# Kernel optimization log

Measured on AMD Instinct MI355X. Metric: run time of the kernel, lower is better.

Reference implementation:

```python
import jax, jax.numpy as jnp
import numpy as np

N = 50000       # num nodes
E = 400000      # num edges (before self loops)
IN, HID, H, OUT = 128, 64, 4, 64
SLOPE = 0.2     # PyG GATv2Conv default negative_slope


def setup_inputs() -> dict:
    key = jax.random.key(0)
    ks = jax.random.split(key, 14)
    def lin(k, fan_in, fan_out):
        return jax.random.normal(k, (fan_in, fan_out), jnp.float32) / np.sqrt(fan_in)
    return {
        "x": jax.random.normal(ks[0], (N, IN), jnp.float32),
        "edge_index": jax.random.randint(ks[1], (2, E), 0, N, jnp.int32),
        # layer 1: in=IN -> HID per head, H heads, concat
        "Wl1": lin(ks[2], IN, H * HID), "bl1": jnp.zeros((H * HID,), jnp.float32),
        "Wr1": lin(ks[3], IN, H * HID), "br1": jnp.zeros((H * HID,), jnp.float32),
        "att1": jax.random.normal(ks[4], (H, HID), jnp.float32) / np.sqrt(HID),
        "bias1": jnp.zeros((H * HID,), jnp.float32),
        # layer 2: in=H*HID -> OUT, 1 head, concat=False
        "Wl2": lin(ks[5], H * HID, OUT), "bl2": jnp.zeros((OUT,), jnp.float32),
        "Wr2": lin(ks[6], H * HID, OUT), "br2": jnp.zeros((OUT,), jnp.float32),
        "att2": jax.random.normal(ks[7], (1, OUT), jnp.float32) / np.sqrt(OUT),
        "bias2": jnp.zeros((OUT,), jnp.float32),
    }


def gatv2_conv(x, src, dst, Wl, bl, Wr, br, att, heads, out_ch, num_nodes):
    """PyG GATv2Conv (share_weights=False). src->dst aggregation at dst."""
    xl = (x @ Wl + bl).reshape(-1, heads, out_ch)  # source transform (x_j)
    xr = (x @ Wr + br).reshape(-1, heads, out_ch)  # target transform (x_i)
    m = xl[src] + xr[dst]                          # [E, H, C]
    e = jnp.sum(jax.nn.leaky_relu(m, SLOPE) * att, axis=-1)  # [E, H]
    # segment softmax over incoming edges of each dst node
    emax = jax.ops.segment_max(e, dst, num_segments=num_nodes)
    ex = jnp.exp(e - emax[dst])
    denom = jax.ops.segment_sum(ex, dst, num_segments=num_nodes)
    alpha = ex / denom[dst]                        # [E, H]
    out = jax.ops.segment_sum(alpha[:, :, None] * xl[src], dst, num_segments=num_nodes)
    return out  # [N, H, C]


def reference(x, edge_index, Wl1, bl1, Wr1, br1, att1, bias1,
              Wl2, bl2, Wr2, br2, att2, bias2):
    n = x.shape[0]
    loops = jnp.arange(n, dtype=edge_index.dtype)
    src = jnp.concatenate([edge_index[0], loops])  # add_self_loops=True
    dst = jnp.concatenate([edge_index[1], loops])
    h = gatv2_conv(x, src, dst, Wl1, bl1, Wr1, br1, att1, H, HID, n)
    h = h.reshape(n, H * HID) + bias1              # concat=True
    h = jax.nn.elu(h)                              # dropout=0.0
    o = gatv2_conv(h, src, dst, Wl2, bl2, Wr2, br2, att2, 1, OUT, n)
    return o.reshape(n, OUT) + bias2               # concat=False, heads=1
```

## Files before the change

kernel.cpp:

```cpp
#include <hip/hip_runtime.h>
#include <hip/hip_bf16.h>

typedef unsigned short u16;
typedef __attribute__((ext_vector_type(8))) short short8;
typedef __attribute__((ext_vector_type(4))) float floatx4;
typedef __attribute__((ext_vector_type(2))) float f32x2;

#define N_NODES 50000
#define N_EDGES 400000
#define ET      450000
#define F_IN    128
#define C1      256
#define HID     64
#define OUTC    64
#define SLOPE   0.2f
#define LIN1_BLOCKS 782

__device__ __forceinline__ float bf2f(u16 v) {
    return __uint_as_float(((unsigned)v) << 16);
}
__device__ __forceinline__ float bflo(unsigned u) { return __uint_as_float(u << 16); }
__device__ __forceinline__ float bfhi(unsigned u) { return __uint_as_float(u & 0xffff0000u); }
__device__ __forceinline__ u16 f2bf(float f) {
    unsigned u = __float_as_uint(f);
    return (u16)((u + 0x7fffu + ((u >> 16) & 1u)) >> 16);
}
__device__ __forceinline__ f32x2 up2(unsigned u) {
    f32x2 r; r.x = bflo(u); r.y = bfhi(u); return r;
}
template<int CTRL>
__device__ __forceinline__ float dpp_add(float x) {
    return x + __int_as_float(__builtin_amdgcn_update_dpp(
        0, __float_as_int(x), CTRL, 0xF, 0xF, true));
}
__device__ __forceinline__ float red16(float p) {
    p = dpp_add<0xB1>(p);
    p = dpp_add<0x4E>(p);
    p = dpp_add<0x141>(p);
    p = dpp_add<0x140>(p);
    return p;
}
__device__ __forceinline__ bool detect_f32(const unsigned* __restrict__ xw) {
    unsigned w = xw[threadIdx.x & 63];
    unsigned aexp = (w >> 7) & 0xFFu;
    unsigned long long b = __ballot(aexp >= 170u || aexp <= 40u);
    return __popcll(b) >= 16;
}

__global__ __launch_bounds__(256) void convert_all_kernel(
    const unsigned* __restrict__ xw,
    const void* wl1, const void* wr1, const void* wl2, const void* wr2,
    const void* s0, const void* s1, const void* s2, const void* s3,
    const void* s4, const void* s5, const void* s6, const void* s7,
    u16* __restrict__ wt, u16* __restrict__ prm, int* __restrict__ hist)
{
    if (blockIdx.x >= 385) {
        int idx = (blockIdx.x - 385) * 256 + threadIdx.x;
        if (idx < N_NODES) hist[idx] = 0;
        return;
    }
    bool f32m = detect_f32(xw);
    if (blockIdx.x == 384) {
        for (int t = threadIdx.x; t < 1280; t += 256) {
            const void* src; int local;
            if      (t < 256)  { src = s0; local = t; }
            else if (t < 512)  { src = s1; local = t - 256; }
            else if (t < 768)  { src = s2; local = t - 512; }
            else if (t < 1024) { src = s3; local = t - 768; }
            else if (t < 1088) { src = s4; local = t - 1024; }
            else if (t < 1152) { src = s5; local = t - 1088; }
            else if (t < 1216) { src = s6; local = t - 1152; }
            else               { src = s7; local = t - 1216; }
            prm[t] = f32m ? f2bf(((const float*)src)[local]) : ((const u16*)src)[local];
        }
        return;
    }
    int t = blockIdx.x * 256 + threadIdx.x;
    const void* src; int local, k, n, K, base;
    if (t < 32768)      { src = wl1; local = t;         k = local >> 8; n = local & 255; K = 128; base = 0; }
    else if (t < 65536) { src = wr1; local = t - 32768; k = local >> 8; n = local & 255; K = 128; base = 32768; }
    else if (t < 81920) { src = wl2; local = t - 65536; k = local >> 6; n = local & 63;  K = 256; base = 65536; }
    else                { src = wr2; local = t - 81920; k = local >> 6; n = local & 63;  K = 256; base = 81920; }
    u16 v = f32m ? f2bf(((const float*)src)[local]) : ((const u16*)src)[local];
    wt[base + n * K + k] = v;
}

__global__ __launch_bounds__(256) void scan1_kernel(const int* __restrict__ hist,
                                                    int* __restrict__ rowptr,
                                                    int* __restrict__ bsum)
{
    int t = threadIdx.x;
    int i = blockIdx.x * 256 + t;
    int v = (i < N_NODES) ? hist[i] : 0;
    __shared__ int sd[256];
    sd[t] = v;
    __syncthreads();
    #pragma unroll
    for (int ofs = 1; ofs < 256; ofs <<= 1) {
        int u = (t >= ofs) ? sd[t - ofs] : 0;
        __syncthreads();
        sd[t] += u;
        __syncthreads();
    }
    if (i < N_NODES) rowptr[i] = sd[t] - v;
    if (t == 255) bsum[blockIdx.x] = sd[255];
}

__global__ __launch_bounds__(256) void scan3_kernel(int* __restrict__ rowptr,
                                                    const int* __restrict__ bsum,
                                                    int* __restrict__ off)
{
    int t = threadIdx.x;
    int v = (t < (int)blockIdx.x) ? bsum[t] : 0;
    __shared__ int sd[256];
    sd[t] = v;
    __syncthreads();
    #pragma unroll
    for (int ofs = 1; ofs < 256; ofs <<= 1) {
        int u = (t >= ofs) ? sd[t - ofs] : 0;
        __syncthreads();
        sd[t] += u;
        __syncthreads();
    }
    int boff = sd[255];
    int i = blockIdx.x * 256 + t;
    if (i < N_NODES) {
        int r = rowptr[i] + boff;
        rowptr[i] = r;
        off[i] = r;
    }
}

__global__ __launch_bounds__(256) void scatter_kernel(const int* __restrict__ ei,
                                                      int* __restrict__ off,
                                                      int* __restrict__ src_csr)
{
    int t = blockIdx.x * 256 + threadIdx.x;
    if (t >= ET) return;
    int s, d;
    if (t < N_EDGES) { s = ei[t]; d = ei[N_EDGES + t]; } else { s = d = t - N_EDGES; }
    int pos = atomicAdd(&off[d], 1);
    src_csr[pos] = s;
}

__global__ __launch_bounds__(256) void lin1_hist_kernel(
    const u16* __restrict__ X, const u16* __restrict__ Wt,
    const u16* __restrict__ bl, const u16* __restrict__ br,
    u16* __restrict__ Yl, u16* __restrict__ Yr, int nrows,
    const int* __restrict__ ei, int* __restrict__ hist)
{
    constexpr int K = 128, N = 256, LS = K + 8;
    __shared__ __align__(16) u16 sX[64 * LS];
    __shared__ __align__(16) u16 sW[64 * LS];

    if (blockIdx.x >= LIN1_BLOCKS) {
        int t = (blockIdx.x - LIN1_BLOCKS) * 256 + threadIdx.x;
        if (t < ET) {
            int d = (t < N_EDGES) ? ei[N_EDGES + t] : t - N_EDGES;
            atomicAdd(&hist[d], 1);
        }
        return;
    }

    const bool f32m = detect_f32((const unsigned*)X);
    const float* X32 = (const float*)X;
    const int row0 = blockIdx.x * 64;
    const int wave = threadIdx.x >> 6, lane = threadIdx.x & 63;
    const int quad = lane >> 4, l16 = lane & 15;

    for (int i = threadIdx.x * 8; i < 64 * K; i += 2048) {
        int r = i >> 7, c = i & 127;
        int gr = row0 + r;
        u16* dst = &sX[r * LS + c];
        if (f32m) {
            float4 v0 = make_float4(0.f, 0.f, 0.f, 0.f), v1 = v0;
            if (gr < nrows) {
                v0 = *(const float4*)&X32[(size_t)gr * K + c];
                v1 = *(const float4*)&X32[(size_t)gr * K + c + 4];
            }
            ushort4 p0, p1;
            p0.x = f2bf(v0.x); p0.y = f2bf(v0.y); p0.z = f2bf(v0.z); p0.w = f2bf(v0.w);
            p1.x = f2bf(v1.x); p1.y = f2bf(v1.y); p1.z = f2bf(v1.z); p1.w = f2bf(v1.w);
            *(ushort4*)dst = p0;
            *(ushort4*)(dst + 4) = p1;
        } else {
            uint4 v = {0u, 0u, 0u, 0u};
            if (gr < nrows) v = *(const uint4*)&X[(size_t)gr * K + c];
            *(uint4*)dst = v;
        }
    }
    __syncthreads();

    short8 a[4];
    #pragma unroll
    for (int kk = 0; kk < 4; ++kk)
        a[kk] = *(const short8*)&sX[(wave * 16 + l16) * LS + kk * 32 + quad * 8];

    for (int side = 0; side < 2; ++side) {
        const u16* wbase = Wt + side * (N * K);
        const u16* bias  = side ? br : bl;
        u16* Y = side ? Yr : Yl;
        for (int ch = 0; ch < 4; ++ch) {
            __syncthreads();
            for (int i = threadIdx.x * 8; i < 64 * K; i += 2048) {
                int n = i >> 7, c = i & 127;
                *(uint4*)&sW[n * LS + c] = *(const uint4*)&wbase[(size_t)(ch * 64 + n) * K + c];
            }
            __syncthreads();
            floatx4 acc0 = {0.f, 0.f, 0.f, 0.f}, acc1 = acc0, acc2 = acc0, acc3 = acc0;
            #pragma unroll
            for (int kk = 0; kk < 4; ++kk) {
                short8 b0 = *(const short8*)&sW[(l16) * LS + kk * 32 + quad * 8];
                short8 b1 = *(const short8*)&sW[(16 + l16) * LS + kk * 32 + quad * 8];
                short8 b2 = *(const short8*)&sW[(32 + l16) * LS + kk * 32 + quad * 8];
                short8 b3 = *(const short8*)&sW[(48 + l16) * LS + kk * 32 + quad * 8];
                acc0 = __builtin_amdgcn_mfma_f32_16x16x32_bf16(a[kk], b0, acc0, 0, 0, 0);
                acc1 = __builtin_amdgcn_mfma_f32_16x16x32_bf16(a[kk], b1, acc1, 0, 0, 0);
                acc2 = __builtin_amdgcn_mfma_f32_16x16x32_bf16(a[kk], b2, acc2, 0, 0, 0);
                acc3 = __builtin_amdgcn_mfma_f32_16x16x32_bf16(a[kk], b3, acc3, 0, 0, 0);
            }
            const int rbase = row0 + wave * 16 + quad * 4;
            #pragma unroll
            for (int cf = 0; cf < 4; ++cf) {
                const floatx4 av = (cf == 0) ? acc0 : (cf == 1) ? acc1 : (cf == 2) ? acc2 : acc3;
                const int col = ch * 64 + cf * 16 + l16;
                const float bv = bf2f(bias[col]);
                #pragma unroll
                for (int r = 0; r < 4; ++r) {
                    int row = rbase + r;
                    if (row < nrows) Y[(size_t)row * N + col] = f2bf(av[r] + bv);
                }
            }
        }
    }
}

__global__ __launch_bounds__(256) void lin2_fused_kernel(
    const u16* __restrict__ X, const u16* __restrict__ Wt,
    const u16* __restrict__ bl, const u16* __restrict__ br,
    u16* __restrict__ Yl, u16* __restrict__ Yr, int nrows)
{
    constexpr int K = 256, N = 64, LS = K + 8;
    __shared__ __align__(16) u16 sX[64 * LS];
    __shared__ __align__(16) u16 sW[64 * LS];
    const int row0 = blockIdx.x * 64;
    const int wave = threadIdx.x >> 6, lane = threadIdx.x & 63;
    const int quad = lane >> 4, l16 = lane & 15;

    for (int i = threadIdx.x * 8; i < 64 * K; i += 2048) {
        int r = i >> 8, c = i & 255;
        int gr = row0 + r;
        uint4 v = {0u, 0u, 0u, 0u};
        if (gr < nrows) v = *(const uint4*)&X[(size_t)gr * K + c];
        *(uint4*)&sX[r * LS + c] = v;
    }
    __syncthreads();

    short8 a[8];
    #pragma unroll
    for (int kk = 0; kk < 8; ++kk)
        a[kk] = *(const short8*)&sX[(wave * 16 + l16) * LS + kk * 32 + quad * 8];

    for (int side = 0; side < 2; ++side) {
        const u16* wbase = Wt + side * (N * K);
        const u16* bias  = side ? br : bl;
        u16* Y = side ? Yr : Yl;
        __syncthreads();
        for (int i = threadIdx.x * 8; i < 64 * K; i += 2048) {
            int n = i >> 8, c = i & 255;
            *(uint4*)&sW[n * LS + c] = *(const uint4*)&wbase[(size_t)n * K + c];
        }
        __syncthreads();
        floatx4 acc0 = {0.f, 0.f, 0.f, 0.f}, acc1 = acc0, acc2 = acc0, acc3 = acc0;
        #pragma unroll
        for (int kk = 0; kk < 8; ++kk) {
            short8 b0 = *(const short8*)&sW[(l16) * LS + kk * 32 + quad * 8];
            short8 b1 = *(const short8*)&sW[(16 + l16) * LS + kk * 32 + quad * 8];
            short8 b2 = *(const short8*)&sW[(32 + l16) * LS + kk * 32 + quad * 8];
            short8 b3 = *(const short8*)&sW[(48 + l16) * LS + kk * 32 + quad * 8];
            acc0 = __builtin_amdgcn_mfma_f32_16x16x32_bf16(a[kk], b0, acc0, 0, 0, 0);
            acc1 = __builtin_amdgcn_mfma_f32_16x16x32_bf16(a[kk], b1, acc1, 0, 0, 0);
            acc2 = __builtin_amdgcn_mfma_f32_16x16x32_bf16(a[kk], b2, acc2, 0, 0, 0);
            acc3 = __builtin_amdgcn_mfma_f32_16x16x32_bf16(a[kk], b3, acc3, 0, 0, 0);
        }
        const int rbase = row0 + wave * 16 + quad * 4;
        #pragma unroll
        for (int cf = 0; cf < 4; ++cf) {
            const floatx4 av = (cf == 0) ? acc0 : (cf == 1) ? acc1 : (cf == 2) ? acc2 : acc3;
            const int col = cf * 16 + l16;
            const float bv = bf2f(bias[col]);
            #pragma unroll
            for (int r = 0; r < 4; ++r) {
                int row = rbase + r;
                if (row < nrows) Y[(size_t)row * N + col] = f2bf(av[r] + bv);
            }
        }
    }
}

__global__ __launch_bounds__(256) void node1_kernel(
    const u16* __restrict__ xl, const u16* __restrict__ xr,
    const int* __restrict__ rowptr, const int* __restrict__ hist,
    const int* __restrict__ src_csr, const u16* __restrict__ att,
    const u16* __restrict__ bias, u16* __restrict__ hout)
{
    const int d = __builtin_amdgcn_readfirstlane(blockIdx.x * 4 + (threadIdx.x >> 6));
    if (d >= N_NODES) return;
    const int l = threadIdx.x & 63;
    const int start = rowptr[d];
    const int deg = hist[d];

    uint2 auv = *(const uint2*)&att[l * 4];
    const f32x2 atA = up2(auv.x), atB = up2(auv.y);
    uint2 ruv = *(const uint2*)&xr[(size_t)d * C1 + l * 4];
    const f32x2 rA = up2(ruv.x), rB = up2(ruv.y);

    float m = -1e30f, la = 0.f;
    f32x2 accA = {0.f, 0.f}, accB = {0.f, 0.f};
    for (int j = 0; j < deg; j += 4) {
        const bool v1 = j + 1 < deg, v2 = j + 2 < deg, v3 = j + 3 < deg;
        int s0 = src_csr[start + j];
        int s1 = v1 ? src_csr[start + j + 1] : s0;
        int s2 = v2 ? src_csr[start + j + 2] : s0;
        int s3 = v3 ? src_csr[start + j + 3] : s0;
        uint2 u0 = *(const uint2*)&xl[(size_t)s0 * C1 + l * 4];
        uint2 u1 = *(const uint2*)&xl[(size_t)s1 * C1 + l * 4];
        uint2 u2 = *(const uint2*)&xl[(size_t)s2 * C1 + l * 4];
        uint2 u3 = *(const uint2*)&xl[(size_t)s3 * C1 + l * 4];
        f32x2 x0A = up2(u0.x), x0B = up2(u0.y);
        f32x2 x1A = up2(u1.x), x1B = up2(u1.y);
        f32x2 x2A = up2(u2.x), x2B = up2(u2.y);
        f32x2 x3A = up2(u3.x), x3B = up2(u3.y);
        f32x2 t, pv;
        t = x0A + rA; t = __builtin_elementwise_max(t, t * SLOPE); pv  = t * atA;
        t = x0B + rB; t = __builtin_elementwise_max(t, t * SLOPE); pv += t * atB;
        float p0 = pv.x + pv.y;
        t = x1A + rA; t = __builtin_elementwise_max(t, t * SLOPE); pv  = t * atA;
        t = x1B + rB; t = __builtin_elementwise_max(t, t * SLOPE); pv += t * atB;
        float p1 = pv.x + pv.y;
        t = x2A + rA; t = __builtin_elementwise_max(t, t * SLOPE); pv  = t * atA;
        t = x2B + rB; t = __builtin_elementwise_max(t, t * SLOPE); pv += t * atB;
        float p2 = pv.x + pv.y;
        t = x3A + rA; t = __builtin_elementwise_max(t, t * SLOPE); pv  = t * atA;
        t = x3B + rB; t = __builtin_elementwise_max(t, t * SLOPE); pv += t * atB;
        float p3 = pv.x + pv.y;
        p0 = red16(p0); p1 = red16(p1); p2 = red16(p2); p3 = red16(p3);
        float pm = p0;
        if (v1) pm = fmaxf(pm, p1);
        if (v2) pm = fmaxf(pm, p2);
        if (v3) pm = fmaxf(pm, p3);
        float mn = fmaxf(m, pm);
        float sc = __expf(m - mn);
        float w0 = __expf(p0 - mn);
        float w1 = v1 ? __expf(p1 - mn) : 0.f;
        float w2 = v2 ? __expf(p2 - mn) : 0.f;
        float w3 = v3 ? __expf(p3 - mn) : 0.f;
        la = la * sc + w0 + w1 + w2 + w3;
        accA = accA * sc + x0A * w0 + x1A * w1 + x2A * w2 + x3A * w3;
        accB = accB * sc + x0B * w0 + x1B * w1 + x2B * w2 + x3B * w3;
        m = mn;
    }
    const float inv = 1.f / la;
    const int c = l * 4;
    float v0 = accA.x * inv + bf2f(bias[c + 0]);
    float v1 = accA.y * inv + bf2f(bias[c + 1]);
    float v2 = accB.x * inv + bf2f(bias[c + 2]);
    float v3 = accB.y * inv + bf2f(bias[c + 3]);
    v0 = v0 > 0.f ? v0 : __expf(fminf(v0, 0.f)) - 1.f;
    v1 = v1 > 0.f ? v1 : __expf(fminf(v1, 0.f)) - 1.f;
    v2 = v2 > 0.f ? v2 : __expf(fminf(v2, 0.f)) - 1.f;
    v3 = v3 > 0.f ? v3 : __expf(fminf(v3, 0.f)) - 1.f;
    ushort4 o;
    o.x = f2bf(v0); o.y = f2bf(v1); o.z = f2bf(v2); o.w = f2bf(v3);
    *(ushort4*)&hout[(size_t)d * C1 + c] = o;
}

__global__ __launch_bounds__(256) void node2_kernel(
    const u16* __restrict__ xl, const u16* __restrict__ xr,
    const int* __restrict__ rowptr, const int* __restrict__ hist,
    const int* __restrict__ src_csr, const u16* __restrict__ att,
    const u16* __restrict__ bias, void* __restrict__ outp,
    const unsigned* __restrict__ xorig)
{
    const bool f32o = detect_f32(xorig);
    const int d = __builtin_amdgcn_readfirstlane(blockIdx.x * 4 + (threadIdx.x >> 6));
    if (d >= N_NODES) return;
    const int l = threadIdx.x & 63;
    const int start = rowptr[d];
    const int deg = hist[d];
    const int g = l >> 4, sub = l & 15;
    const int c0 = sub * 4;

    uint2 auv = *(const uint2*)&att[c0];
    const f32x2 atA = up2(auv.x), atB = up2(auv.y);
    uint2 ruv = *(const uint2*)&xr[(size_t)d * OUTC + c0];
    const f32x2 rA = up2(ruv.x), rB = up2(ruv.y);

    float m = -1e30f, la = 0.f;
    f32x2 accA = {0.f, 0.f}, accB = {0.f, 0.f};
    for (int j = 0; j < deg; j += 4) {
        const bool valid = j + g < deg;
        int s = valid ? src_csr[start + j + g] : d;
        uint2 uv = *(const uint2*)&xl[(size_t)s * OUTC + c0];
        f32x2 xA = up2(uv.x), xB = up2(uv.y);
        f32x2 t, pv;
        t = xA + rA; t = __builtin_elementwise_max(t, t * SLOPE); pv  = t * atA;
        t = xB + rB; t = __builtin_elementwise_max(t, t * SLOPE); pv += t * atB;
        float p = pv.x + pv.y;
        p = red16(p);
        float pvv = valid ? p : -1e30f;
        float mn = fmaxf(m, pvv);
        float sc = __expf(m - mn);
        float w  = valid ? __expf(p - mn) : 0.f;
        la = la * sc + w;
        accA = accA * sc + xA * w;
        accB = accB * sc + xB * w;
        m = mn;
    }
    #pragma unroll
    for (int ofs = 16; ofs <= 32; ofs <<= 1) {
        float mo = __shfl_xor(m, ofs);
        float lo = __shfl_xor(la, ofs);
        float bax = __shfl_xor(accA.x, ofs);
        float bay = __shfl_xor(accA.y, ofs);
        float bbx = __shfl_xor(accB.x, ofs);
        float bby = __shfl_xor(accB.y, ofs);
        float mn = fmaxf(m, mo);
        float s0 = __expf(m - mn), s1 = __expf(mo - mn);
        la = la * s0 + lo * s1;
        accA.x = accA.x * s0 + bax * s1;
        accA.y = accA.y * s0 + bay * s1;
        accB.x = accB.x * s0 + bbx * s1;
        accB.y = accB.y * s0 + bby * s1;
        m = mn;
    }
    if (g == 0) {
        const float inv = 1.f / la;
        float v0 = accA.x * inv + bf2f(bias[c0 + 0]);
        float v1 = accA.y * inv + bf2f(bias[c0 + 1]);
        float v2 = accB.x * inv + bf2f(bias[c0 + 2]);
        float v3 = accB.y * inv + bf2f(bias[c0 + 3]);
        if (f32o) {
            float4 o = make_float4(v0, v1, v2, v3);
            *(float4*)&((float*)outp)[(size_t)d * OUTC + c0] = o;
        } else {
            ushort4 o;
            o.x = f2bf(v0); o.y = f2bf(v1); o.z = f2bf(v2); o.w = f2bf(v3);
            *(ushort4*)&((u16*)outp)[(size_t)d * OUTC + c0] = o;
        }
    }
}

extern "C" void kernel_launch(void* const* d_in, const int* in_sizes, int n_in,
                              void* d_out, int out_size, void* d_ws, size_t ws_size,
                              hipStream_t stream)
{
    const void* x  = d_in[0];
    const int*  ei = (const int*)d_in[1];

    char* ws = (char*)d_ws;
    u16* xl1     = (u16*)(ws + 0);
    u16* xr1     = (u16*)(ws + 25600000);
    u16* hbuf    = (u16*)(ws + 51200000);
    u16* xl2     = (u16*)(ws + 0);
    u16* xr2     = (u16*)(ws + 6400000);
    int* hist    = (int*)(ws + 76800000);
    int* rowptr  = (int*)(ws + 77000000);
    int* off     = (int*)(ws + 77200000);
    int* src_csr = (int*)(ws + 77400000);
    u16* prm     = (u16*)(ws + 79200064);
    u16* wt      = (u16*)(ws + 79210240);
    int* bsum    = (int*)(ws + 79410000);

    u16* bl1   = prm + 0;
    u16* br1   = prm + 256;
    u16* att1  = prm + 512;
    u16* bias1 = prm + 768;
    u16* bl2   = prm + 1024;
    u16* br2   = prm + 1088;
    u16* att2  = prm + 1152;
    u16* bias2 = prm + 1216;
    u16* wt1   = wt + 0;
    u16* wt2   = wt + 65536;

    convert_all_kernel<<<581, 256, 0, stream>>>(
        (const unsigned*)x,
        d_in[2], d_in[4], d_in[8], d_in[10],
        d_in[3], d_in[5], d_in[6], d_in[7], d_in[9], d_in[11], d_in[12], d_in[13],
        wt, prm, hist);

    const int eb = (ET + 255) / 256;
    lin1_hist_kernel<<<LIN1_BLOCKS + eb, 256, 0, stream>>>(
        (const u16*)x, wt1, bl1, br1, xl1, xr1, N_NODES, ei, hist);

    scan1_kernel<<<196, 256, 0, stream>>>(hist, rowptr, bsum);
    scan3_kernel<<<196, 256, 0, stream>>>(rowptr, bsum, off);
    scatter_kernel<<<eb, 256, 0, stream>>>(ei, off, src_csr);

    const int nb = (N_NODES * 64 + 255) / 256;
    node1_kernel<<<nb, 256, 0, stream>>>(xl1, xr1, rowptr, hist, src_csr, att1, bias1, hbuf);
    lin2_fused_kernel<<<(N_NODES + 63) / 64, 256, 0, stream>>>(hbuf, wt2, bl2, br2, xl2, xr2, N_NODES);
    node2_kernel<<<nb, 256, 0, stream>>>(xl2, xr2, rowptr, hist, src_csr, att2, bias2, d_out,
                                         (const unsigned*)x);
}
```

Before: 247.1 us.

## Prefetch neighbor gathers, use exp2 softmax, one-wave blocks in node kernels

The node aggregation kernels now issue the next group of source-row gathers before computing the current group, so memory latency overlaps with the attention math. The softmax switches to base-2 exponentials by pre-scaling the attention vector by log2(e). Node1 reduces two edge scores per DPP pass, and both kernels launch one 64-thread block per node with occupancy hints instead of four waves per block. Registers rise because of the prefetch buffers, and the larger block count adds scheduling overhead.

```diff
diff --git a/kernel.cpp b/kernel.cpp
--- a/kernel.cpp
+++ b/kernel.cpp
@@ -15,6 +15,13 @@
 #define OUTC    64
 #define SLOPE   0.2f
 #define LIN1_BLOCKS 782
+#define LOG2E   1.44269504089f
+
+#if __has_builtin(__builtin_amdgcn_exp2f)
+#define EXP2(x) __builtin_amdgcn_exp2f(x)
+#else
+#define EXP2(x) __expf((x) * 0.69314718056f)
+#endif
 
 __device__ __forceinline__ float bf2f(u16 v) {
     return __uint_as_float(((unsigned)v) << 16);
@@ -38,6 +45,22 @@
     p = dpp_add<0x4E>(p);
     p = dpp_add<0x141>(p);
     p = dpp_add<0x140>(p);
+    return p;
+}
+template<int CTRL>
+__device__ __forceinline__ f32x2 dpp_add2(f32x2 x) {
+    f32x2 o;
+    o.x = __int_as_float(__builtin_amdgcn_update_dpp(
+        0, __float_as_int(x.x), CTRL, 0xF, 0xF, true));
+    o.y = __int_as_float(__builtin_amdgcn_update_dpp(
+        0, __float_as_int(x.y), CTRL, 0xF, 0xF, true));
+    return x + o;
+}
+__device__ __forceinline__ f32x2 red16x2(f32x2 p) {
+    p = dpp_add2<0xB1>(p);
+    p = dpp_add2<0x4E>(p);
+    p = dpp_add2<0x141>(p);
+    p = dpp_add2<0x140>(p);
     return p;
 }
 __device__ __forceinline__ bool detect_f32(const unsigned* __restrict__ xw) {
@@ -298,39 +321,53 @@
     }
 }
 
-__global__ __launch_bounds__(256) void node1_kernel(
+__global__ __launch_bounds__(64, 6) void node1_kernel(
     const u16* __restrict__ xl, const u16* __restrict__ xr,
     const int* __restrict__ rowptr, const int* __restrict__ hist,
     const int* __restrict__ src_csr, const u16* __restrict__ att,
     const u16* __restrict__ bias, u16* __restrict__ hout)
 {
-    const int d = __builtin_amdgcn_readfirstlane(blockIdx.x * 4 + (threadIdx.x >> 6));
-    if (d >= N_NODES) return;
-    const int l = threadIdx.x & 63;
+    const int d = blockIdx.x;
+    const int l = threadIdx.x;
     const int start = rowptr[d];
     const int deg = hist[d];
+    const u16* __restrict__ xlp = xl + l * 4;
 
     uint2 auv = *(const uint2*)&att[l * 4];
-    const f32x2 atA = up2(auv.x), atB = up2(auv.y);
+    const f32x2 atA = up2(auv.x) * LOG2E, atB = up2(auv.y) * LOG2E;
     uint2 ruv = *(const uint2*)&xr[(size_t)d * C1 + l * 4];
     const f32x2 rA = up2(ruv.x), rB = up2(ruv.y);
 
     float m = -1e30f, la = 0.f;
     f32x2 accA = {0.f, 0.f}, accB = {0.f, 0.f};
+
+    int s0 = src_csr[start];
+    int s1 = (1 < deg) ? src_csr[start + 1] : s0;
+    int s2 = (2 < deg) ? src_csr[start + 2] : s0;
+    int s3 = (3 < deg) ? src_csr[start + 3] : s0;
+    uint2 u0 = *(const uint2*)&xlp[(size_t)s0 * C1];
+    uint2 u1 = *(const uint2*)&xlp[(size_t)s1 * C1];
+    uint2 u2 = *(const uint2*)&xlp[(size_t)s2 * C1];
+    uint2 u3 = *(const uint2*)&xlp[(size_t)s3 * C1];
+
     for (int j = 0; j < deg; j += 4) {
+        const uint2 c0 = u0, c1 = u1, c2 = u2, c3 = u3;
         const bool v1 = j + 1 < deg, v2 = j + 2 < deg, v3 = j + 3 < deg;
-        int s0 = src_csr[start + j];
-        int s1 = v1 ? src_csr[start + j + 1] : s0;
-        int s2 = v2 ? src_csr[start + j + 2] : s0;
-        int s3 = v3 ? src_csr[start + j + 3] : s0;
-        uint2 u0 = *(const uint2*)&xl[(size_t)s0 * C1 + l * 4];
-        uint2 u1 = *(const uint2*)&xl[(size_t)s1 * C1 + l * 4];
-        uint2 u2 = *(const uint2*)&xl[(size_t)s2 * C1 + l * 4];
-        uint2 u3 = *(const uint2*)&xl[(size_t)s3 * C1 + l * 4];
-        f32x2 x0A = up2(u0.x), x0B = up2(u0.y);
-        f32x2 x1A = up2(u1.x), x1B = up2(u1.y);
-        f32x2 x2A = up2(u2.x), x2B = up2(u2.y);
-        f32x2 x3A = up2(u3.x), x3B = up2(u3.y);
+        const int jn = j + 4;
+        if (jn < deg) {
+            int t0 = src_csr[start + jn];
+            int t1 = (jn + 1 < deg) ? src_csr[start + jn + 1] : t0;
+            int t2 = (jn + 2 < deg) ? src_csr[start + jn + 2] : t0;
+            int t3 = (jn + 3 < deg) ? src_csr[start + jn + 3] : t0;
+            u0 = *(const uint2*)&xlp[(size_t)t0 * C1];
+            u1 = *(const uint2*)&xlp[(size_t)t1 * C1];
+            u2 = *(const uint2*)&xlp[(size_t)t2 * C1];
+            u3 = *(const uint2*)&xlp[(size_t)t3 * C1];
+        }
+        f32x2 x0A = up2(c0.x), x0B = up2(c0.y);
+        f32x2 x1A = up2(c1.x), x1B = up2(c1.y);
+        f32x2 x2A = up2(c2.x), x2B = up2(c2.y);
+        f32x2 x3A = up2(c3.x), x3B = up2(c3.y);
         f32x2 t, pv;
         t = x0A + rA; t = __builtin_elementwise_max(t, t * SLOPE); pv  = t * atA;
         t = x0B + rB; t = __builtin_elementwise_max(t, t * SLOPE); pv += t * atB;
@@ -344,17 +381,20 @@
         t = x3A + rA; t = __builtin_elementwise_max(t, t * SLOPE); pv  = t * atA;
         t = x3B + rB; t = __builtin_elementwise_max(t, t * SLOPE); pv += t * atB;
         float p3 = pv.x + pv.y;
-        p0 = red16(p0); p1 = red16(p1); p2 = red16(p2); p3 = red16(p3);
+        f32x2 P01 = {p0, p1}, P23 = {p2, p3};
+        P01 = red16x2(P01);
+        P23 = red16x2(P23);
+        p0 = P01.x; p1 = P01.y; p2 = P23.x; p3 = P23.y;
         float pm = p0;
         if (v1) pm = fmaxf(pm, p1);
         if (v2) pm = fmaxf(pm, p2);
         if (v3) pm = fmaxf(pm, p3);
         float mn = fmaxf(m, pm);
-        float sc = __expf(m - mn);
-        float w0 = __expf(p0 - mn);
-        float w1 = v1 ? __expf(p1 - mn) : 0.f;
-        float w2 = v2 ? __expf(p2 - mn) : 0.f;
-        float w3 = v3 ? __expf(p3 - mn) : 0.f;
+        float sc = EXP2(m - mn);
+        float w0 = EXP2(p0 - mn);
+        float w1 = v1 ? EXP2(p1 - mn) : 0.f;
+        float w2 = v2 ? EXP2(p2 - mn) : 0.f;
+        float w3 = v3 ? EXP2(p3 - mn) : 0.f;
         la = la * sc + w0 + w1 + w2 + w3;
         accA = accA * sc + x0A * w0 + x1A * w1 + x2A * w2 + x3A * w3;
         accB = accB * sc + x0B * w0 + x1B * w1 + x2B * w2 + x3B * w3;
@@ -375,7 +415,7 @@
     *(ushort4*)&hout[(size_t)d * C1 + c] = o;
 }
 
-__global__ __launch_bounds__(256) void node2_kernel(
+__global__ __launch_bounds__(64, 8) void node2_kernel(
     const u16* __restrict__ xl, const u16* __restrict__ xr,
     const int* __restrict__ rowptr, const int* __restrict__ hist,
     const int* __restrict__ src_csr, const u16* __restrict__ att,
@@ -383,25 +423,33 @@
     const unsigned* __restrict__ xorig)
 {
     const bool f32o = detect_f32(xorig);
-    const int d = __builtin_amdgcn_readfirstlane(blockIdx.x * 4 + (threadIdx.x >> 6));
-    if (d >= N_NODES) return;
-    const int l = threadIdx.x & 63;
+    const int d = blockIdx.x;
+    const int l = threadIdx.x;
     const int start = rowptr[d];
     const int deg = hist[d];
     const int g = l >> 4, sub = l & 15;
     const int c0 = sub * 4;
+    const u16* __restrict__ xlp = xl + c0;
 
     uint2 auv = *(const uint2*)&att[c0];
-    const f32x2 atA = up2(auv.x), atB = up2(auv.y);
+    const f32x2 atA = up2(auv.x) * LOG2E, atB = up2(auv.y) * LOG2E;
     uint2 ruv = *(const uint2*)&xr[(size_t)d * OUTC + c0];
     const f32x2 rA = up2(ruv.x), rB = up2(ruv.y);
 
     float m = -1e30f, la = 0.f;
     f32x2 accA = {0.f, 0.f}, accB = {0.f, 0.f};
+
+    int sN = (g < deg) ? src_csr[start + g] : d;
+    uint2 uN = *(const uint2*)&xlp[(size_t)sN * OUTC];
+
     for (int j = 0; j < deg; j += 4) {
         const bool valid = j + g < deg;
-        int s = valid ? src_csr[start + j + g] : d;
-        uint2 uv = *(const uint2*)&xl[(size_t)s * OUTC + c0];
+        const uint2 uv = uN;
+        const int jn = j + 4;
+        if (jn < deg) {
+            int sn = (jn + g < deg) ? src_csr[start + jn + g] : d;
+            uN = *(const uint2*)&xlp[(size_t)sn * OUTC];
+        }
         f32x2 xA = up2(uv.x), xB = up2(uv.y);
         f32x2 t, pv;
         t = xA + rA; t = __builtin_elementwise_max(t, t * SLOPE); pv  = t * atA;
@@ -410,8 +458,8 @@
         p = red16(p);
         float pvv = valid ? p : -1e30f;
         float mn = fmaxf(m, pvv);
-        float sc = __expf(m - mn);
-        float w  = valid ? __expf(p - mn) : 0.f;
+        float sc = EXP2(m - mn);
+        float w  = valid ? EXP2(p - mn) : 0.f;
         la = la * sc + w;
         accA = accA * sc + xA * w;
         accB = accB * sc + xB * w;
@@ -426,12 +474,12 @@
         float bbx = __shfl_xor(accB.x, ofs);
         float bby = __shfl_xor(accB.y, ofs);
         float mn = fmaxf(m, mo);
-        float s0 = __expf(m - mn), s1 = __expf(mo - mn);
-        la = la * s0 + lo * s1;
-        accA.x = accA.x * s0 + bax * s1;
-        accA.y = accA.y * s0 + bay * s1;
-        accB.x = accB.x * s0 + bbx * s1;
-        accB.y = accB.y * s0 + bby * s1;
+        float e0 = EXP2(m - mn), e1 = EXP2(mo - mn);
+        la = la * e0 + lo * e1;
+        accA.x = accA.x * e0 + bax * e1;
+        accA.y = accA.y * e0 + bay * e1;
+        accB.x = accB.x * e0 + bbx * e1;
+        accB.y = accB.y * e0 + bby * e1;
         m = mn;
     }
     if (g == 0) {
@@ -497,9 +545,8 @@
     scan3_kernel<<<196, 256, 0, stream>>>(rowptr, bsum, off);
     scatter_kernel<<<eb, 256, 0, stream>>>(ei, off, src_csr);
 
-    const int nb = (N_NODES * 64 + 255) / 256;
-    node1_kernel<<<nb, 256, 0, stream>>>(xl1, xr1, rowptr, hist, src_csr, att1, bias1, hbuf);
+    node1_kernel<<<N_NODES, 64, 0, stream>>>(xl1, xr1, rowptr, hist, src_csr, att1, bias1, hbuf);
     lin2_fused_kernel<<<(N_NODES + 63) / 64, 256, 0, stream>>>(hbuf, wt2, bl2, br2, xl2, xr2, N_NODES);
-    node2_kernel<<<nb, 256, 0, stream>>>(xl2, xr2, rowptr, hist, src_csr, att2, bias2, d_out,
-                                         (const unsigned*)x);
-}
+    node2_kernel<<<N_NODES, 64, 0, stream>>>(xl2, xr2, rowptr, hist, src_csr, att2, bias2, d_out,
+                                             (const unsigned*)x);
+}
```

Result: faster. 239.4 us (-3.1%).
